# Optimization experiments

Measured on AMD Instinct MI355X. Metric: run time of the kernel, lower is better.

## Reference

```python
import jax, jax.numpy as jnp
import numpy as np

V, D, H, M, E, K = 32000, 1024, 1024, 64, 8, 2
B, S = 2, 2048


def _w(k, shape):
    fan_in = shape[-2] if len(shape) > 1 else shape[-1]
    return (jax.random.normal(k, shape, jnp.float32) / np.sqrt(fan_in)).astype(jnp.float32)


def setup_inputs() -> dict:
    key = jax.random.key(0)
    ks = jax.random.split(key, 24)
    HE = H // 2  # expert hidden = 512
    return {
        "input_ids": jax.random.randint(ks[0], (B, S), 0, V, dtype=jnp.int64),
        "emb": _w(ks[1], (V, D)),
        "enc_W": _w(ks[2], (D, H)), "enc_b": jnp.zeros((H,), jnp.float32),
        "s2c_W": _w(ks[3], (H, M)), "s2c_b": jnp.zeros((M,), jnp.float32),
        "rW1": _w(ks[4], (M, 64)), "rb1": jnp.zeros((64,), jnp.float32),
        "rW2": _w(ks[5], (64, E)), "rb2": jnp.zeros((E,), jnp.float32),
        "eW1": _w(ks[6], (E, M, HE)), "eb1": jnp.zeros((E, HE), jnp.float32),
        "eW2": _w(ks[7], (E, HE, M)), "eb2": jnp.zeros((E, M), jnp.float32),
        "c2s_W": _w(ks[8], (M, H)), "c2s_b": jnp.zeros((H,), jnp.float32),
        "dec_W": _w(ks[9], (H, D)), "dec_b": jnp.zeros((D,), jnp.float32),
        "out_W": _w(ks[10], (D, V)), "out_b": jnp.zeros((V,), jnp.float32),
    }


def reference(input_ids, emb, enc_W, enc_b, s2c_W, s2c_b, rW1, rb1, rW2, rb2,
              eW1, eb1, eW2, eb2, c2s_W, c2s_b, dec_W, dec_b, out_W, out_b):
    b, s = input_ids.shape
    n = b * s
    num_e = rW2.shape[1]
    # 1) embed + GIF encoder (linear + sigmoid spike-rate surrogate)
    x = emb[input_ids]                                   # (B,S,D)
    spikes_enc = jax.nn.sigmoid(x @ enc_W + enc_b)       # (B,S,H)
    # 2) spike -> continuous (rate coding over time window, then linear)
    cont = spikes_enc.reshape(n, -1) @ s2c_W + s2c_b     # (N,M)
    # 3) liquid MoE router: tanh MLP gate, softmax, top-k, renormalize
    gate_h = jnp.tanh(cont @ rW1 + rb1)
    probs = jax.nn.softmax(gate_h @ rW2 + rb2, axis=-1)  # (N,E)
    topv, topi = jax.lax.top_k(probs, K)                 # (N,K)
    wts = topv / jnp.sum(topv, axis=-1, keepdims=True)
    # per-token dense combine weights (zero for unselected experts) — matches
    # the original mask-and-sum over the full expert loop
    w_full = jnp.zeros((n, num_e), cont.dtype).at[jnp.arange(n)[:, None], topi].add(wts)
    # 4) all experts on all tokens (as in the source loop), then weighted combine
    h1 = jax.nn.relu(jnp.einsum('nm,emh->enh', cont, eW1) + eb1[:, None, :])  # (E,N,H/2)
    eo = jnp.einsum('enh,ehm->enm', h1, eW2) + eb2[:, None, :]                # (E,N,M)
    expert_out = jnp.einsum('ne,enm->nm', w_full, eo)                         # (N,M)
    # 5) continuous -> spike (Poisson expected rate) then time-average
    spikes_moe = jax.nn.sigmoid(expert_out @ c2s_W + c2s_b)                   # (N,H)
    spikes_avg = spikes_moe.reshape(b, s, -1)                                 # (B,S,H)
    # 6) GIF decoder + output projection
    decoded = jax.nn.sigmoid(spikes_avg @ dec_W + dec_b)                      # (B,S,D)
    logits = decoded @ out_W + out_b                                          # (B,S,V)
    return (logits, probs.reshape(b, s, num_e))
```

## Files before the change

kernel.cpp:

```cpp
#include <hip/hip_runtime.h>
#include <hip/hip_bf16.h>
#include <math.h>


typedef __bf16 bf16x8 __attribute__((ext_vector_type(8)));
typedef float f32x4 __attribute__((ext_vector_type(4)));

__device__ __forceinline__ ushort f2bf(float f) {
  union { float f; unsigned u; } v; v.f = f;
  unsigned u = v.u;
  u += 0x7FFFu + ((u >> 16) & 1u);
  return (ushort)(u >> 16);
}

__device__ __forceinline__ void async16(const void* g, void* l) {
  __builtin_amdgcn_global_load_lds((const __attribute__((address_space(1))) void*)g,
                                   (__attribute__((address_space(3))) void*)l,
                                   16, 0, 0);
}

__global__ void pack_w_kernel(const float* __restrict__ W, ushort* __restrict__ Wpk,
                              int K, int N) {
  long t = (long)blockIdx.x * blockDim.x + threadIdx.x;
  long total = (long)(K >> 3) * N;
  if (t >= total) return;
  long kb = t / N;
  int n = (int)(t - kb * N);
  long zoff = (long)blockIdx.y * K * N;
  const float* src = W + zoff + (kb * 8) * (long)N + n;
  union { ushort u[8]; uint4 v; } o;
#pragma unroll
  for (int j = 0; j < 8; ++j) o.u[j] = f2bf(src[(long)j * N]);
  *(uint4*)(Wpk + zoff + t * 8) = o.v;
}

__global__ void embed_pk_kernel(const int* __restrict__ ids, const float* __restrict__ emb,
                                ushort* __restrict__ xpk, int M) {
  int m = blockIdx.x * blockDim.x + threadIdx.x;
  int kb = blockIdx.y;
  long id = ids[m];
  const float4* s = (const float4*)(emb + id * 1024 + kb * 8);
  float4 a = s[0], b = s[1];
  union { ushort u[8]; uint4 v; } o;
  o.u[0] = f2bf(a.x); o.u[1] = f2bf(a.y); o.u[2] = f2bf(a.z); o.u[3] = f2bf(a.w);
  o.u[4] = f2bf(b.x); o.u[5] = f2bf(b.y); o.u[6] = f2bf(b.z); o.u[7] = f2bf(b.w);
  *(uint4*)(xpk + ((size_t)kb * M + m) * 8) = o.v;
}

template <int WAVES_M, int WAVES_N, int WM, int WN, int ACT, int OUT>
__launch_bounds__(WAVES_M * WAVES_N * 64)
__global__ void gemm_pk(const ushort* __restrict__ A, const ushort* __restrict__ B,
                        const float* __restrict__ bias, void* __restrict__ Cout,
                        int M, int N, int K, long sA, long sB, long sBias, long sC) {
  constexpr int BM = WAVES_M * WM * 16;
  constexpr int BN = WAVES_N * WN * 16;
  constexpr int NW = WAVES_M * WAVES_N;
  constexpr int ACH = 8 * BM / 64;
  constexpr int BCH = 8 * BN / 64;

  __shared__ ushort As[8 * BM * 8];
  __shared__ ushort Bs[8 * BN * 8];

  const int tid = threadIdx.x;
  const int lane = tid & 63;
  const int wave = tid >> 6;
  const int wm = wave % WAVES_M;
  const int wn = wave / WAVES_M;
  const int m0 = blockIdx.x * BM;
  const int n0 = blockIdx.y * BN;
  const int z = blockIdx.z;

  A += (size_t)z * sA;
  B += (size_t)z * sB;
  const float* biasp = bias + (size_t)z * sBias;

  f32x4 acc[WM][WN] = {};

  const int ktiles = K >> 6;
  const int q = lane >> 4;
  const int r16 = lane & 15;

  for (int kt = 0; kt < ktiles; ++kt) {
    const int kb0 = kt * 8;
#pragma unroll
    for (int c = wave; c < ACH; c += NW) {
      int kb = c / (BM / 64);
      int hh = c % (BM / 64);
      const ushort* g = A + (((size_t)(kb0 + kb)) * M + m0 + hh * 64 + lane) * 8;
      ushort* l = &As[(kb * BM + hh * 64) * 8];
      async16(g, l);
    }
#pragma unroll
    for (int c = wave; c < BCH; c += NW) {
      int kb = c / (BN / 64);
      int hh = c % (BN / 64);
      const ushort* g = B + (((size_t)(kb0 + kb)) * N + n0 + hh * 64 + lane) * 8;
      ushort* l = &Bs[(kb * BN + hh * 64) * 8];
      async16(g, l);
    }
    __syncthreads();
#pragma unroll
    for (int kk = 0; kk < 2; ++kk) {
      bf16x8 a[WM], b[WN];
#pragma unroll
      for (int mt = 0; mt < WM; ++mt)
        a[mt] = *(const bf16x8*)&As[((kk * 4 + q) * BM + wm * WM * 16 + mt * 16 + r16) * 8];
#pragma unroll
      for (int nt = 0; nt < WN; ++nt)
        b[nt] = *(const bf16x8*)&Bs[((kk * 4 + q) * BN + wn * WN * 16 + nt * 16 + r16) * 8];
#pragma unroll
      for (int mt = 0; mt < WM; ++mt)
#pragma unroll
        for (int nt = 0; nt < WN; ++nt)
          acc[mt][nt] = __builtin_amdgcn_mfma_f32_16x16x32_bf16(a[mt], b[nt], acc[mt][nt], 0, 0, 0);
    }
    __syncthreads();
  }

#pragma unroll
  for (int mt = 0; mt < WM; ++mt) {
#pragma unroll
    for (int nt = 0; nt < WN; ++nt) {
      int col = n0 + wn * WN * 16 + nt * 16 + r16;
      float bv = biasp[col];
#pragma unroll
      for (int r = 0; r < 4; ++r) {
        int row = m0 + wm * WM * 16 + mt * 16 + q * 4 + r;
        float v = acc[mt][nt][r] + bv;
        if (ACT == 1) v = 1.f / (1.f + expf(-v));
        else if (ACT == 2) v = fmaxf(v, 0.f);
        if (OUT == 0) {
          ((float*)Cout)[(size_t)z * sC + (size_t)row * N + col] = v;
        } else {
          ((ushort*)Cout)[(size_t)z * sC + ((size_t)(col >> 3) * M + row) * 8 + (col & 7)] = f2bf(v);
        }
      }
    }
  }
}


#define SBAR0 __builtin_amdgcn_sched_barrier(0)
#define BARRIER { SBAR0; __builtin_amdgcn_s_barrier(); SBAR0; }
#define PRIO1 __builtin_amdgcn_s_setprio(1)
#define PRIO0 __builtin_amdgcn_s_setprio(0)

template <int Mc, int Nc, int Kc>
__global__ __launch_bounds__(512, 2)
void gemm_out_pipe(const ushort* __restrict__ A, const ushort* __restrict__ B,
                   const float* __restrict__ bias, float* __restrict__ C) {
  static_assert((Kc / 64) >= 4 && (Kc / 64) % 2 == 0, "need even ktiles >= 4");
  extern __shared__ ushort lds[];
  const int tid = threadIdx.x;
  const int lane = tid & 63;
  const int wave = tid >> 6;
  const int wm = wave & 1;
  const int wn = wave >> 1;
  const int q = lane >> 4;
  const int r16 = lane & 15;

  const int cpx = gridDim.x >> 3;
  const int swz = ((int)blockIdx.x & 7) * cpx + ((int)blockIdx.x >> 3);
  constexpr int mtiles = Mc >> 8;
  const int m0 = (swz % mtiles) << 8;
  const int n0 = (swz / mtiles) << 8;

  const int s_kb = wave >> 1;
  const int s_row = ((wave & 1) << 6) + lane;

  f32x4 acc[8][4] = {};
  bf16x8 aE[2][2], aO[2][2], b[4][2];

  auto stageA = [&](int kt, int h, int buf) {
    const ushort* g = A + (size_t)(((kt * 8 + s_kb) * Mc + m0 + h * 128 + s_row) * 8);
    ushort* l = lds + buf * 32768 + (s_kb * 256 + h * 128 + s_row) * 8;
    async16(g, l);
    async16(g + 4 * Mc * 8, l + 4 * 256 * 8);
  };
  auto stageB = [&](int kt, int h, int buf) {
    const ushort* g = B + (size_t)(((kt * 8 + s_kb) * Nc + n0 + h * 128 + s_row) * 8);
    ushort* l = lds + buf * 32768 + 16384 + (s_kb * 256 + h * 128 + s_row) * 8;
    async16(g, l);
    async16(g + 4 * Nc * 8, l + 4 * 256 * 8);
  };
  auto LDA = [&](int buf, int QQ, bf16x8 (&a)[2][2]) {
#pragma unroll
    for (int mi = 0; mi < 2; ++mi)
#pragma unroll
      for (int kk = 0; kk < 2; ++kk)
        a[mi][kk] = *(const bf16x8*)&lds[buf * 32768 +
                                         ((kk * 4 + q) * 256 + wm * 128 + (QQ * 2 + mi) * 16 + r16) * 8];
  };
  auto LDB = [&](int buf) {
#pragma unroll
    for (int nf = 0; nf < 4; ++nf)
#pragma unroll
      for (int kk = 0; kk < 2; ++kk)
        b[nf][kk] = *(const bf16x8*)&lds[buf * 32768 + 16384 +
                                         ((kk * 4 + q) * 256 + wn * 64 + nf * 16 + r16) * 8];
  };
  auto MF = [&](int QQ, bf16x8 (&a)[2][2]) {
#pragma unroll
    for (int kk = 0; kk < 2; ++kk)
#pragma unroll
      for (int mi = 0; mi < 2; ++mi)
#pragma unroll
        for (int nf = 0; nf < 4; ++nf)
          acc[QQ * 2 + mi][nf] =
              __builtin_amdgcn_mfma_f32_16x16x32_bf16(a[mi][kk], b[nf][kk], acc[QQ * 2 + mi][nf], 0, 0, 0);
  };

  constexpr int ktiles = Kc >> 6;

  stageB(0, 0, 0); stageB(0, 1, 0);
  stageA(0, 0, 0); stageA(0, 1, 0);
  stageB(1, 0, 1); stageB(1, 1, 1);
  asm volatile("s_waitcnt vmcnt(4)" ::: "memory");
  BARRIER;
  LDB(0); LDA(0, 0, aE);
  SBAR0;

#define TILE_FULL(T, BUF, OBUF)                               \
  {                                                           \
    LDA(BUF, 1, aO); stageA((T) + 1, 0, OBUF);                \
    SBAR0; PRIO1; MF(0, aE); PRIO0; SBAR0;                    \
    LDA(BUF, 2, aE); stageA((T) + 1, 1, OBUF);                \
    SBAR0; PRIO1; MF(1, aO); PRIO0;                           \
    BARRIER;                                                  \
    LDA(BUF, 3, aO); stageB((T) + 2, 0, BUF);                 \
    SBAR0; PRIO1; MF(2, aE); PRIO0; SBAR0;                    \
    stageB((T) + 2, 1, BUF);                                  \
    SBAR0; PRIO1; MF(3, aO); PRIO0; SBAR0;                    \
    asm volatile("s_waitcnt vmcnt(4)" ::: "memory");          \
    BARRIER;                                                  \
    LDB(OBUF); LDA(OBUF, 0, aE);                              \
    SBAR0;                                                    \
  }

  for (int t = 0; t < ktiles - 2; t += 2) {
    TILE_FULL(t, 0, 1);
    TILE_FULL(t + 1, 1, 0);
  }

  {
    LDA(0, 1, aO); stageA(ktiles - 1, 0, 1);
    SBAR0; PRIO1; MF(0, aE); PRIO0; SBAR0;
    LDA(0, 2, aE); stageA(ktiles - 1, 1, 1);
    SBAR0; PRIO1; MF(1, aO); PRIO0;
    BARRIER;
    LDA(0, 3, aO);
    SBAR0; PRIO1; MF(2, aE); PRIO0; SBAR0;
    PRIO1; MF(3, aO); PRIO0; SBAR0;
    asm volatile("s_waitcnt vmcnt(0)" ::: "memory");
    BARRIER;
    LDB(1); LDA(1, 0, aE);
    SBAR0;
  }
  {
    LDA(1, 1, aO);
    SBAR0; PRIO1; MF(0, aE); PRIO0; SBAR0;
    LDA(1, 2, aE);
    SBAR0; PRIO1; MF(1, aO); PRIO0; SBAR0;
    LDA(1, 3, aO);
    SBAR0; PRIO1; MF(2, aE); PRIO0; SBAR0;
    PRIO1; MF(3, aO); PRIO0;
  }
#undef TILE_FULL

#pragma unroll
  for (int nf = 0; nf < 4; ++nf) {
    const int col = n0 + wn * 64 + nf * 16 + r16;
    const float bv = bias[col];
#pragma unroll
    for (int mf = 0; mf < 8; ++mf) {
      const int row = m0 + wm * 128 + mf * 16 + q * 4;
      float* out = C + (size_t)row * Nc + col;
#pragma unroll
      for (int r = 0; r < 4; ++r)
        out[(size_t)r * Nc] = acc[mf][nf][r] + bv;
    }
  }
}

__global__ void s2c_kernel(const float* __restrict__ spikes, const float* __restrict__ W,
                           const float* __restrict__ b, float* __restrict__ cont,
                           ushort* __restrict__ contpk, int M) {
  int tid = threadIdx.x;
  int m = tid & 63;
  int n = blockIdx.x * 4 + (tid >> 6);
  const float* srow = spikes + (size_t)n * 1024;
  float acc = b[m];
#pragma unroll 8
  for (int k = 0; k < 1024; ++k) acc = fmaf(srow[k], W[k * 64 + m], acc);
  cont[(size_t)n * 64 + m] = acc;
  contpk[((size_t)(m >> 3) * M + n) * 8 + (m & 7)] = f2bf(acc);
}

__global__ void router_kernel(const float* __restrict__ cont, const float* __restrict__ rW1,
                              const float* __restrict__ rb1, const float* __restrict__ rW2,
                              const float* __restrict__ rb2, float* __restrict__ probs,
                              float* __restrict__ wfull) {
  int n = blockIdx.x;
  int L = threadIdx.x;
  float c = cont[(size_t)n * 64 + L];
  float gh = rb1[L];
#pragma unroll 8
  for (int k = 0; k < 64; ++k) {
    float ck = __shfl(c, k, 64);
    gh = fmaf(ck, rW1[k * 64 + L], gh);
  }
  gh = tanhf(gh);
  __shared__ float ghs[64];
  ghs[L] = gh;
  __syncthreads();
  float lg = 0.f;
  if (L < 8) {
    lg = rb2[L];
#pragma unroll 8
    for (int h = 0; h < 64; ++h) lg = fmaf(ghs[h], rW2[h * 8 + L], lg);
  }
  float mx = lg;
  for (int o = 4; o >= 1; o >>= 1) mx = fmaxf(mx, __shfl_xor(mx, o, 8));
  float ex = expf(lg - mx);
  float sm = ex;
  for (int o = 4; o >= 1; o >>= 1) sm += __shfl_xor(sm, o, 8);
  float pr = ex / sm;
  __shared__ float ps[8];
  if (L < 8) { probs[(size_t)n * 8 + L] = pr; ps[L] = pr; }
  __syncthreads();
  if (L == 0) {
    int i1 = 0; float v1 = ps[0];
#pragma unroll
    for (int e = 1; e < 8; ++e) if (ps[e] > v1) { v1 = ps[e]; i1 = e; }
    float v2 = -1.f; int i2 = 0;
#pragma unroll
    for (int e = 0; e < 8; ++e) if (e != i1 && ps[e] > v2) { v2 = ps[e]; i2 = e; }
    float s = v1 + v2;
    float w[8];
#pragma unroll
    for (int e = 0; e < 8; ++e) w[e] = 0.f;
    w[i1] = v1 / s; w[i2] = v2 / s;
#pragma unroll
    for (int e = 0; e < 8; ++e) wfull[(size_t)n * 8 + e] = w[e];
  }
}

__global__ void combine_kernel(const float* __restrict__ eo, const float* __restrict__ wfull,
                               ushort* __restrict__ exopk, int M) {
  int t = blockIdx.x * 256 + threadIdx.x;
  int n = t >> 6, m = t & 63;
  float acc = 0.f;
#pragma unroll
  for (int e = 0; e < 8; ++e)
    acc = fmaf(wfull[(size_t)n * 8 + e], eo[((size_t)e * M + n) * 64 + m], acc);
  exopk[((size_t)(m >> 3) * M + n) * 8 + (m & 7)] = f2bf(acc);
}

extern "C" void kernel_launch(void* const* d_in, const int* in_sizes, int n_in,
                              void* d_out, int out_size, void* d_ws, size_t ws_size,
                              hipStream_t stream) {
  const int*   ids   = (const int*)  d_in[0];
  const float* emb   = (const float*)d_in[1];
  const float* enc_W = (const float*)d_in[2];
  const float* enc_b = (const float*)d_in[3];
  const float* s2c_W = (const float*)d_in[4];
  const float* s2c_b = (const float*)d_in[5];
  const float* rW1   = (const float*)d_in[6];
  const float* rb1   = (const float*)d_in[7];
  const float* rW2   = (const float*)d_in[8];
  const float* rb2   = (const float*)d_in[9];
  const float* eW1   = (const float*)d_in[10];
  const float* eb1   = (const float*)d_in[11];
  const float* eW2   = (const float*)d_in[12];
  const float* eb2   = (const float*)d_in[13];
  const float* c2s_W = (const float*)d_in[14];
  const float* c2s_b = (const float*)d_in[15];
  const float* dec_W = (const float*)d_in[16];
  const float* dec_b = (const float*)d_in[17];
  const float* out_W = (const float*)d_in[18];
  const float* out_b = (const float*)d_in[19];
  (void)in_sizes; (void)n_in; (void)out_size; (void)ws_size;

  const int M = 4096, D = 1024, H = 1024, Mm = 64, E = 8, V = 32000, HE = 512;

  char* p = (char*)d_ws;
  auto alloc = [&](size_t bytes) { void* r = (void*)p; p += (bytes + 255) & ~(size_t)255; return r; };
  ushort* xpk    = (ushort*)alloc((size_t)M * D * 2);
  ushort* encWpk = (ushort*)alloc((size_t)D * H * 2);
  float*  spikes = (float*) alloc((size_t)M * H * 4);
  float*  cont   = (float*) alloc((size_t)M * Mm * 4);
  ushort* contpk = (ushort*)alloc((size_t)M * Mm * 2);
  float*  wfull  = (float*) alloc((size_t)M * E * 4);
  ushort* eW1pk  = (ushort*)alloc((size_t)E * Mm * HE * 2);
  ushort* eW2pk  = (ushort*)alloc((size_t)E * HE * Mm * 2);
  ushort* h1pk   = (ushort*)alloc((size_t)E * M * HE * 2);
  float*  eo     = (float*) alloc((size_t)E * M * Mm * 4);
  ushort* exopk  = (ushort*)alloc((size_t)M * Mm * 2);
  ushort* c2sWpk = (ushort*)alloc((size_t)Mm * H * 2);
  ushort* smoepk = (ushort*)alloc((size_t)M * H * 2);
  ushort* decWpk = (ushort*)alloc((size_t)H * D * 2);
  ushort* decpk  = (ushort*)alloc((size_t)M * D * 2);
  ushort* outWpk = (ushort*)alloc((size_t)D * V * 2);

  float* logits = (float*)d_out;
  float* probs  = logits + (size_t)M * V;

  static bool attr_done = false;
  if (!attr_done) {
    (void)hipFuncSetAttribute(reinterpret_cast<const void*>(&gemm_out_pipe<4096, 32000, 1024>),
                              hipFuncAttributeMaxDynamicSharedMemorySize, 131072);
    attr_done = true;
  }

  pack_w_kernel<<<dim3(((D / 8) * H + 255) / 256, 1), 256, 0, stream>>>(enc_W, encWpk, D, H);
  pack_w_kernel<<<dim3(((Mm / 8) * HE + 255) / 256, E), 256, 0, stream>>>(eW1, eW1pk, Mm, HE);
  pack_w_kernel<<<dim3(((HE / 8) * Mm + 255) / 256, E), 256, 0, stream>>>(eW2, eW2pk, HE, Mm);
  pack_w_kernel<<<dim3(((Mm / 8) * H + 255) / 256, 1), 256, 0, stream>>>(c2s_W, c2sWpk, Mm, H);
  pack_w_kernel<<<dim3(((H / 8) * D + 255) / 256, 1), 256, 0, stream>>>(dec_W, decWpk, H, D);
  pack_w_kernel<<<dim3(((D / 8) * V + 255) / 256, 1), 256, 0, stream>>>(out_W, outWpk, D, V);

  embed_pk_kernel<<<dim3(M / 256, D / 8), 256, 0, stream>>>(ids, emb, xpk, M);
  gemm_pk<2, 2, 4, 4, 1, 0><<<dim3(M / 128, H / 128, 1), 256, 0, stream>>>(
      xpk, encWpk, enc_b, spikes, M, H, D, 0, 0, 0, 0);
  s2c_kernel<<<dim3(M / 4), 256, 0, stream>>>(spikes, s2c_W, s2c_b, cont, contpk, M);
  router_kernel<<<dim3(M), 64, 0, stream>>>(cont, rW1, rb1, rW2, rb2, probs, wfull);
  gemm_pk<2, 2, 4, 4, 2, 1><<<dim3(M / 128, HE / 128, E), 256, 0, stream>>>(
      contpk, eW1pk, eb1, h1pk, M, HE, Mm, 0, (long)Mm * HE, HE, (long)M * HE);
  gemm_pk<4, 1, 2, 4, 0, 0><<<dim3(M / 128, 1, E), 256, 0, stream>>>(
      h1pk, eW2pk, eb2, eo, M, Mm, HE, (long)M * HE, (long)HE * Mm, Mm, (long)M * Mm);
  combine_kernel<<<dim3(M * Mm / 256), 256, 0, stream>>>(eo, wfull, exopk, M);
  gemm_pk<2, 2, 4, 4, 1, 1><<<dim3(M / 128, H / 128, 1), 256, 0, stream>>>(
      exopk, c2sWpk, c2s_b, smoepk, M, H, Mm, 0, 0, 0, 0);
  gemm_pk<2, 2, 4, 4, 1, 1><<<dim3(M / 128, D / 128, 1), 256, 0, stream>>>(
      smoepk, decWpk, dec_b, decpk, M, D, H, 0, 0, 0, 0);
  gemm_out_pipe<4096, 32000, 1024><<<dim3((M / 256) * (V / 256)), 512, 131072, stream>>>(
      decpk, outWpk, out_b, logits);
}
```

Measured before the change: 1.129 ms.

## Triple-buffer A tiles and prefetch two k-tiles ahead in output GEMM

Restructures the LM-head GEMM pipeline so the A operand uses three LDS buffers and B uses two. Both operands are now prefetched two k-tiles ahead, and the loop runs one tile per iteration with rotating buffer indices instead of a two-tile unrolled macro. Dynamic LDS grows from 128KB to 160KB, and the wait threshold changes to vmcnt(8). The aim is to hide more global-load latency behind MFMA work. The cost is using the full LDS budget and runtime-computed buffer offsets.

Result: no change. 1.140 ms (+0.9%).

```diff
diff --git a/kernel.cpp b/kernel.cpp
--- a/kernel.cpp
+++ b/kernel.cpp
@@ -149,7 +149,7 @@
 __global__ __launch_bounds__(512, 2)
 void gemm_out_pipe(const ushort* __restrict__ A, const ushort* __restrict__ B,
                    const float* __restrict__ bias, float* __restrict__ C) {
-  static_assert((Kc / 64) >= 4 && (Kc / 64) % 2 == 0, "need even ktiles >= 4");
+  static_assert((Kc / 64) >= 4, "need ktiles >= 4");
   extern __shared__ ushort lds[];
   const int tid = threadIdx.x;
   const int lane = tid & 63;
@@ -171,32 +171,32 @@
   f32x4 acc[8][4] = {};
   bf16x8 aE[2][2], aO[2][2], b[4][2];
 
-  auto stageA = [&](int kt, int h, int buf) {
+  auto stageA = [&](int kt, int h, int ab) {
     const ushort* g = A + (size_t)(((kt * 8 + s_kb) * Mc + m0 + h * 128 + s_row) * 8);
-    ushort* l = lds + buf * 32768 + (s_kb * 256 + h * 128 + s_row) * 8;
+    ushort* l = lds + ab * 16384 + (s_kb * 256 + h * 128 + s_row) * 8;
     async16(g, l);
     async16(g + 4 * Mc * 8, l + 4 * 256 * 8);
   };
-  auto stageB = [&](int kt, int h, int buf) {
+  auto stageB = [&](int kt, int h, int bbuf) {
     const ushort* g = B + (size_t)(((kt * 8 + s_kb) * Nc + n0 + h * 128 + s_row) * 8);
-    ushort* l = lds + buf * 32768 + 16384 + (s_kb * 256 + h * 128 + s_row) * 8;
+    ushort* l = lds + 49152 + bbuf * 16384 + (s_kb * 256 + h * 128 + s_row) * 8;
     async16(g, l);
     async16(g + 4 * Nc * 8, l + 4 * 256 * 8);
   };
-  auto LDA = [&](int buf, int QQ, bf16x8 (&a)[2][2]) {
+  auto LDA = [&](int ab, int QQ, bf16x8 (&a)[2][2]) {
 #pragma unroll
     for (int mi = 0; mi < 2; ++mi)
 #pragma unroll
       for (int kk = 0; kk < 2; ++kk)
-        a[mi][kk] = *(const bf16x8*)&lds[buf * 32768 +
+        a[mi][kk] = *(const bf16x8*)&lds[ab * 16384 +
                                          ((kk * 4 + q) * 256 + wm * 128 + (QQ * 2 + mi) * 16 + r16) * 8];
   };
-  auto LDB = [&](int buf) {
+  auto LDB = [&](int bbuf) {
 #pragma unroll
     for (int nf = 0; nf < 4; ++nf)
 #pragma unroll
       for (int kk = 0; kk < 2; ++kk)
-        b[nf][kk] = *(const bf16x8*)&lds[buf * 32768 + 16384 +
+        b[nf][kk] = *(const bf16x8*)&lds[49152 + bbuf * 16384 +
                                          ((kk * 4 + q) * 256 + wn * 64 + nf * 16 + r16) * 8];
   };
   auto MF = [&](int QQ, bf16x8 (&a)[2][2]) {
@@ -211,61 +211,62 @@
   };
 
   constexpr int ktiles = Kc >> 6;
-
+  int abR = 0;
+  int bb = 0;
+
+  stageA(0, 0, 0); stageA(0, 1, 0);
   stageB(0, 0, 0); stageB(0, 1, 0);
-  stageA(0, 0, 0); stageA(0, 1, 0);
+  stageA(1, 0, 1); stageA(1, 1, 1);
   stageB(1, 0, 1); stageB(1, 1, 1);
-  asm volatile("s_waitcnt vmcnt(4)" ::: "memory");
+  asm volatile("s_waitcnt vmcnt(8)" ::: "memory");
   BARRIER;
   LDB(0); LDA(0, 0, aE);
   SBAR0;
 
-#define TILE_FULL(T, BUF, OBUF)                               \
-  {                                                           \
-    LDA(BUF, 1, aO); stageA((T) + 1, 0, OBUF);                \
-    SBAR0; PRIO1; MF(0, aE); PRIO0; SBAR0;                    \
-    LDA(BUF, 2, aE); stageA((T) + 1, 1, OBUF);                \
-    SBAR0; PRIO1; MF(1, aO); PRIO0;                           \
-    BARRIER;                                                  \
-    LDA(BUF, 3, aO); stageB((T) + 2, 0, BUF);                 \
-    SBAR0; PRIO1; MF(2, aE); PRIO0; SBAR0;                    \
-    stageB((T) + 2, 1, BUF);                                  \
-    SBAR0; PRIO1; MF(3, aO); PRIO0; SBAR0;                    \
-    asm volatile("s_waitcnt vmcnt(4)" ::: "memory");          \
-    BARRIER;                                                  \
-    LDB(OBUF); LDA(OBUF, 0, aE);                              \
-    SBAR0;                                                    \
-  }
-
-  for (int t = 0; t < ktiles - 2; t += 2) {
-    TILE_FULL(t, 0, 1);
-    TILE_FULL(t + 1, 1, 0);
+  for (int t = 0; t < ktiles - 2; ++t) {
+    const int abW = (abR >= 1) ? abR - 1 : 2;
+    LDA(abR, 1, aO);
+    SBAR0; PRIO1; MF(0, aE); PRIO0;
+    BARRIER;
+    stageB(t + 2, 0, bb); stageB(t + 2, 1, bb);
+    LDA(abR, 2, aE);
+    SBAR0; PRIO1; MF(1, aO); PRIO0; SBAR0;
+    stageA(t + 2, 0, abW); stageA(t + 2, 1, abW);
+    LDA(abR, 3, aO);
+    SBAR0; PRIO1; MF(2, aE); PRIO0; SBAR0;
+    PRIO1; MF(3, aO); PRIO0; SBAR0;
+    asm volatile("s_waitcnt vmcnt(8)" ::: "memory");
+    BARRIER;
+    abR = (abR == 2) ? 0 : abR + 1;
+    bb ^= 1;
+    LDB(bb); LDA(abR, 0, aE);
+    SBAR0;
   }
 
   {
-    LDA(0, 1, aO); stageA(ktiles - 1, 0, 1);
+    LDA(abR, 1, aO);
     SBAR0; PRIO1; MF(0, aE); PRIO0; SBAR0;
-    LDA(0, 2, aE); stageA(ktiles - 1, 1, 1);
-    SBAR0; PRIO1; MF(1, aO); PRIO0;
-    BARRIER;
-    LDA(0, 3, aO);
+    LDA(abR, 2, aE);
+    SBAR0; PRIO1; MF(1, aO); PRIO0; SBAR0;
+    LDA(abR, 3, aO);
     SBAR0; PRIO1; MF(2, aE); PRIO0; SBAR0;
     PRIO1; MF(3, aO); PRIO0; SBAR0;
     asm volatile("s_waitcnt vmcnt(0)" ::: "memory");
     BARRIER;
-    LDB(1); LDA(1, 0, aE);
+    abR = (abR == 2) ? 0 : abR + 1;
+    bb ^= 1;
+    LDB(bb); LDA(abR, 0, aE);
     SBAR0;
   }
   {
-    LDA(1, 1, aO);
+    LDA(abR, 1, aO);
     SBAR0; PRIO1; MF(0, aE); PRIO0; SBAR0;
-    LDA(1, 2, aE);
+    LDA(abR, 2, aE);
     SBAR0; PRIO1; MF(1, aO); PRIO0; SBAR0;
-    LDA(1, 3, aO);
+    LDA(abR, 3, aO);
     SBAR0; PRIO1; MF(2, aE); PRIO0; SBAR0;
     PRIO1; MF(3, aO); PRIO0;
   }
-#undef TILE_FULL
 
 #pragma unroll
   for (int nf = 0; nf < 4; ++nf) {
@@ -408,7 +409,7 @@
   static bool attr_done = false;
   if (!attr_done) {
     (void)hipFuncSetAttribute(reinterpret_cast<const void*>(&gemm_out_pipe<4096, 32000, 1024>),
-                              hipFuncAttributeMaxDynamicSharedMemorySize, 131072);
+                              hipFuncAttributeMaxDynamicSharedMemorySize, 163840);
     attr_done = true;
   }
 
@@ -433,6 +434,6 @@
       exopk, c2sWpk, c2s_b, smoepk, M, H, Mm, 0, 0, 0, 0);
   gemm_pk<2, 2, 4, 4, 1, 1><<<dim3(M / 128, D / 128, 1), 256, 0, stream>>>(
       smoepk, decWpk, dec_b, decpk, M, D, H, 0, 0, 0, 0);
-  gemm_out_pipe<4096, 32000, 1024><<<dim3((M / 256) * (V / 256)), 512, 131072, stream>>>(
+  gemm_out_pipe<4096, 32000, 1024><<<dim3((M / 256) * (V / 256)), 512, 163840, stream>>>(
       decpk, outWpk, out_b, logits);
 }
```
